# Kernel tuning notes

Hardware: AMD Instinct MI355X
Metric: run time of the kernel (lower is better)

Reference implementation:

```python
import jax, jax.numpy as jnp
import numpy as np

N_NODES = 100000
N_EDGES = 1000000
D = 64            # in_channels == heads*hidden_channels
OUT = 64          # out_channels
L = 3             # local_layers
RVQ = 3           # residual VQ levels per layer
CODES = 16
BN_EPS = 1e-5
COMMIT_W = 0.25


def _l2n(v, eps=1e-12):
    return v / (jnp.linalg.norm(v, axis=-1, keepdims=True) + eps)


def setup_inputs() -> dict:
    key = jax.random.key(0)
    ks = jax.random.split(key, 16)
    s = 1.0 / np.sqrt(D)
    inp = {
        "x": jax.random.normal(ks[0], (N_NODES, D), jnp.float32),
        "edge_index": jax.random.randint(ks[1], (2, N_EDGES), 0, N_NODES, jnp.int64),
        # SAGEConv: lin_l (applied to mean-aggregated neighbors, with bias), lin_r (root, no bias)
        "Wa": jax.random.uniform(ks[2], (L, D, D), jnp.float32, -s, s),
        "ba": jax.random.uniform(ks[3], (L, D), jnp.float32, -s, s),
        "Wr": jax.random.uniform(ks[4], (L, D, D), jnp.float32, -s, s),
        # skip Linear per layer
        "Wl": jax.random.uniform(ks[5], (L, D, D), jnp.float32, -s, s),
        "bl": jax.random.uniform(ks[6], (L, D), jnp.float32, -s, s),
        # BatchNorm affine
        "gamma": jnp.ones((L, D), jnp.float32),
        "beta": jnp.zeros((L, D), jnp.float32),
        # residual-VQ codebooks: [layer, rvq_level, codes, dim]
        "codebooks": jax.random.normal(ks[7], (L, RVQ, CODES, D), jnp.float32),
        # heads
        "Wp": jax.random.uniform(ks[8], (D, OUT), jnp.float32, -s, s),
        "bp": jax.random.uniform(ks[9], (OUT,), jnp.float32, -s, s),
        "Wg": jax.random.uniform(ks[10], (D, L * RVQ), jnp.float32, -s, s),
        "bg": jax.random.uniform(ks[11], (L * RVQ,), jnp.float32, -s, s),
    }
    return inp


def _sage_conv(x, src, dst, Wa, ba, Wr):
    # mean aggregation of source features onto destinations
    summed = jax.ops.segment_sum(x[src], dst, num_segments=N_NODES)
    cnt = jax.ops.segment_sum(jnp.ones((src.shape[0],), x.dtype), dst, num_segments=N_NODES)
    mean = summed / jnp.maximum(cnt, 1.0)[:, None]
    out = mean @ Wa + ba + x @ Wr
    return _l2n(out)  # normalize=True


def _residual_vq(x, cbs):
    # cosine-sim residual VQ, 3 levels; returns (quantized_sum, ids [N,RVQ], commit_loss)
    residual = x
    quant = jnp.zeros_like(x)
    loss = jnp.zeros((), x.dtype)
    ids = []
    for r in range(RVQ):
        cb = _l2n(cbs[r])                       # [CODES, D]
        sim = _l2n(residual) @ cb.T             # [N, CODES]
        idx = jnp.argmax(sim, axis=-1)          # [N]
        q = cb[idx]                             # [N, D]
        loss = loss + COMMIT_W * jnp.mean((jax.lax.stop_gradient(q) - residual) ** 2)
        q_st = residual + jax.lax.stop_gradient(q - residual)  # straight-through
        quant = quant + q_st
        residual = residual - jax.lax.stop_gradient(q)
        ids.append(idx)
    return quant, jnp.stack(ids, axis=1), loss


def reference(x, edge_index, Wa, ba, Wr, Wl, bl, gamma, beta, codebooks, Wp, bp, Wg, bg):
    src, dst = edge_index[0], edge_index[1]
    h = x  # in_dropout: identity at inference
    x_local = jnp.zeros((N_NODES, D), x.dtype)
    total_commit = jnp.zeros((), x.dtype)
    id_list = []
    for i in range(L):
        h = _sage_conv(h, src, dst, Wa[i], ba[i], Wr[i]) + (h @ Wl[i] + bl[i])
        # BatchNorm1d (batch statistics)
        mu = jnp.mean(h, axis=0)
        var = jnp.var(h, axis=0)
        h = (h - mu) * jax.lax.rsqrt(var + BN_EPS) * gamma[i] + beta[i]
        h = jax.nn.relu(h)  # dropout: identity at inference
        x_local = x_local + h
        _, ids, closs = _residual_vq(h, codebooks[i])
        total_commit = total_commit + closs
        id_list.append(ids)
    id_concat = jnp.concatenate(id_list, axis=1)  # [N, L*RVQ]
    gnn_id = x_local @ Wg + bg
    pred = x_local @ Wp + bp
    return (pred, total_commit, id_concat, gnn_id)
```

## Files before the change

### kernel.cpp

```cpp
#include <hip/hip_runtime.h>
#include <math.h>

#define NN 100000
#define NE 1000000
#define D 64
#define L 3
#define RVQ 3
#define CODES 16
#define BN_EPS 1e-5f
#define COMMIT_W 0.25f

#define GRID_A 2048

#define OFS_ROWPTR 0
#define OFS_CNT    100016
#define OFS_CURSOR 200032
#define OFS_BSUMS  300048
#define OFS_BOFFS  300176
#define OFS_STATS  300304
#define OFS_CSR    300800
#define OFS_HA     1300800
#define OFS_HB     7700800
#define OFS_XLOC   14100800
#define OFS_PART   20500800

#define OUT_PRED   0
#define OUT_COMMIT (NN * D)
#define OUT_IDS    (NN * D + 1)
#define OUT_GNN    (NN * D + 1 + NN * (L * RVQ))

static __device__ __forceinline__ float waveSum(float v) {
    #pragma unroll
    for (int off = 32; off; off >>= 1) v += __shfl_xor(v, off, 64);
    return v;
}

__global__ void k_count(const int* __restrict__ dst, int* __restrict__ cnt) {
    int e = blockIdx.x * blockDim.x + threadIdx.x;
    if (e < NE) atomicAdd(&cnt[dst[e]], 1);
}

#define SCAN_B 1024
__global__ void k_scan1(const int* __restrict__ cnt, int* __restrict__ rowptr,
                        int* __restrict__ bsums) {
    __shared__ int sm[SCAN_B];
    int t = threadIdx.x;
    int i = blockIdx.x * SCAN_B + t;
    int v = (i < NN) ? cnt[i] : 0;
    sm[t] = v;
    __syncthreads();
    for (int off = 1; off < SCAN_B; off <<= 1) {
        int add = (t >= off) ? sm[t - off] : 0;
        __syncthreads();
        sm[t] += add;
        __syncthreads();
    }
    if (i < NN) rowptr[i + 1] = sm[t];
    if (t == SCAN_B - 1) bsums[blockIdx.x] = sm[t];
}

__global__ void k_scan2(const int* __restrict__ bsums, int* __restrict__ boffs, int nb) {
    __shared__ int sm[SCAN_B];
    int t = threadIdx.x;
    int orig = (t < nb) ? bsums[t] : 0;
    sm[t] = orig;
    __syncthreads();
    for (int off = 1; off < SCAN_B; off <<= 1) {
        int add = (t >= off) ? sm[t - off] : 0;
        __syncthreads();
        sm[t] += add;
        __syncthreads();
    }
    if (t < nb) boffs[t] = sm[t] - orig;
}

__global__ void k_scan3(int* __restrict__ rowptr, const int* __restrict__ boffs) {
    int i = blockIdx.x * SCAN_B + threadIdx.x;
    if (i < NN) rowptr[i + 1] += boffs[blockIdx.x];
    if (i == 0) rowptr[0] = 0;
}

__global__ void k_cursor(const int* __restrict__ rowptr, int* __restrict__ cursor) {
    int i = blockIdx.x * blockDim.x + threadIdx.x;
    if (i < NN) cursor[i] = rowptr[i];
}

__global__ void k_fill(const int* __restrict__ src, const int* __restrict__ dst,
                       int* __restrict__ cursor, int* __restrict__ csr_src) {
    int e = blockIdx.x * blockDim.x + threadIdx.x;
    if (e < NE) {
        int p = atomicAdd(&cursor[dst[e]], 1);
        csr_src[p] = src[e];
    }
}

__global__ void k_sortrows(const int* __restrict__ rowptr, int* __restrict__ csr) {
    int n = blockIdx.x * blockDim.x + threadIdx.x;
    if (n >= NN) return;
    int r0 = rowptr[n], r1 = rowptr[n + 1];
    for (int i = r0 + 1; i < r1; ++i) {
        int v = csr[i];
        int j = i - 1;
        while (j >= r0 && csr[j] > v) { csr[j + 1] = csr[j]; --j; }
        csr[j + 1] = v;
    }
}

__global__ __launch_bounds__(256) void k_gather(
    const float* __restrict__ h, const int* __restrict__ rowptr,
    const int* __restrict__ csr_src, float* __restrict__ mean_out) {
    int t = threadIdx.x;
    int lane = t & 63, wid = t >> 6;
    int n = blockIdx.x * 4 + wid;
    if (n >= NN) return;

    int r0 = rowptr[n], r1 = rowptr[n + 1];
    float s = 0.f;
    for (int base = r0; base < r1; base += 64) {
        int last = r1 - 1;
        int ii = base + lane;
        int idx = csr_src[(ii <= last) ? ii : last];
        int m = r1 - base;
        if (m > 64) m = 64;
        int j = 0;
        for (; j + 8 <= m; j += 8) {
            int i0 = __shfl(idx, j + 0, 64), i1 = __shfl(idx, j + 1, 64);
            int i2 = __shfl(idx, j + 2, 64), i3 = __shfl(idx, j + 3, 64);
            int i4 = __shfl(idx, j + 4, 64), i5 = __shfl(idx, j + 5, 64);
            int i6 = __shfl(idx, j + 6, 64), i7 = __shfl(idx, j + 7, 64);
            float v0 = h[i0 * D + lane], v1 = h[i1 * D + lane];
            float v2 = h[i2 * D + lane], v3 = h[i3 * D + lane];
            float v4 = h[i4 * D + lane], v5 = h[i5 * D + lane];
            float v6 = h[i6 * D + lane], v7 = h[i7 * D + lane];
            s += v0; s += v1; s += v2; s += v3;
            s += v4; s += v5; s += v6; s += v7;
        }
        for (; j + 4 <= m; j += 4) {
            int i0 = __shfl(idx, j + 0, 64), i1 = __shfl(idx, j + 1, 64);
            int i2 = __shfl(idx, j + 2, 64), i3 = __shfl(idx, j + 3, 64);
            float v0 = h[i0 * D + lane], v1 = h[i1 * D + lane];
            float v2 = h[i2 * D + lane], v3 = h[i3 * D + lane];
            s += v0; s += v1; s += v2; s += v3;
        }
        for (; j < m; ++j) {
            int i0 = __shfl(idx, j, 64);
            s += h[i0 * D + lane];
        }
    }
    float deg = (float)(r1 - r0);
    mean_out[n * D + lane] = s / fmaxf(deg, 1.0f);
}

__global__ __launch_bounds__(256) void k_matvec(
    const float* __restrict__ h, float* __restrict__ hp,
    const float* __restrict__ Wa, const float* __restrict__ ba,
    const float* __restrict__ Wr, const float* __restrict__ Wl,
    const float* __restrict__ bl, float* __restrict__ partials) {
    __shared__ float red[2][4][D];
    __shared__ float lbuf[4][2][128];
    int t = threadIdx.x, lane = t & 63, wid = t >> 6;

    float wa[D], wr[D], wl[D];
    #pragma unroll
    for (int k = 0; k < D; ++k) {
        wa[k] = Wa[k * D + lane];
        wr[k] = Wr[k * D + lane];
        wl[k] = Wl[k * D + lane];
    }
    float bav = ba[lane], blv = bl[lane];

    int wg = blockIdx.x * 4 + wid;
    const int wstep = GRID_A * 4;
    float accS = 0.f, accQ = 0.f;

    int seg = lane >> 4;
    int sl  = lane & 15;

    {
        float4 v = {0.f, 0.f, 0.f, 0.f};
        if (seg == 0)      v = *(const float4*)(hp + (size_t)wg * D + 4 * sl);
        else if (seg == 1) v = *(const float4*)(h  + (size_t)wg * D + 4 * sl);
        if (seg < 2) *(float4*)&lbuf[wid][0][seg * 64 + 4 * sl] = v;
    }

    int p = 0;
    for (int n = wg; n < NN; n += wstep) {
        int nn = n + wstep;
        bool havepf = (nn < NN);
        float4 pf = {0.f, 0.f, 0.f, 0.f};
        if (havepf && seg < 2) {
            const float* srcp = (seg == 0) ? hp : h;
            pf = *(const float4*)(srcp + (size_t)nn * D + 4 * sl);
        }

        const float* mb = &lbuf[wid][p][0];
        const float* hb = &lbuf[wid][p][64];
        float a = 0.f, r = 0.f, lv = 0.f;
        #pragma unroll
        for (int j = 0; j < 16; ++j) {
            float4 m4 = *(const float4*)(mb + 4 * j);
            float4 h4 = *(const float4*)(hb + 4 * j);
            a += m4.x * wa[4 * j + 0]; r += h4.x * wr[4 * j + 0]; lv += h4.x * wl[4 * j + 0];
            a += m4.y * wa[4 * j + 1]; r += h4.y * wr[4 * j + 1]; lv += h4.y * wl[4 * j + 1];
            a += m4.z * wa[4 * j + 2]; r += h4.z * wr[4 * j + 2]; lv += h4.z * wl[4 * j + 2];
            a += m4.w * wa[4 * j + 3]; r += h4.w * wr[4 * j + 3]; lv += h4.w * wl[4 * j + 3];
        }
        float sage = a + bav + r;
        float ss = waveSum(sage * sage);
        float inv = 1.0f / (sqrtf(ss) + 1e-12f);
        float hpv = sage * inv + lv + blv;
        hp[(size_t)n * D + lane] = hpv;
        accS += hpv;
        accQ += hpv * hpv;

        if (havepf && seg < 2)
            *(float4*)&lbuf[wid][p ^ 1][seg * 64 + 4 * sl] = pf;
        p ^= 1;
    }

    red[0][wid][lane] = accS;
    red[1][wid][lane] = accQ;
    __syncthreads();
    if (wid == 0) {
        float s0 = (red[0][0][lane] + red[0][1][lane]) + (red[0][2][lane] + red[0][3][lane]);
        float q0 = (red[1][0][lane] + red[1][1][lane]) + (red[1][2][lane] + red[1][3][lane]);
        partials[blockIdx.x * 128 + lane]      = s0;
        partials[blockIdx.x * 128 + 64 + lane] = q0;
    }
}

__global__ __launch_bounds__(256) void k_red_stats(
    const float* __restrict__ part, float* __restrict__ stats) {
    __shared__ float sm[256];
    int c = blockIdx.x;
    int i = threadIdx.x;
    float s = 0.f;
    #pragma unroll
    for (int k = 0; k < 8; ++k)
        s += part[(size_t)(i * 8 + k) * 128 + c];
    sm[i] = s;
    __syncthreads();
    #pragma unroll
    for (int off = 128; off >= 1; off >>= 1) {
        if (i < off) sm[i] += sm[i + off];
        __syncthreads();
    }
    if (i == 0) stats[c] = sm[0];
}

#define CBSTRIDE 65
__global__ __launch_bounds__(256) void k_layer_b(
    float* __restrict__ hp,
    const float* __restrict__ stats,
    const float* __restrict__ gamma, const float* __restrict__ beta,
    const float* __restrict__ cbs,
    float* __restrict__ x_local,
    float* __restrict__ ids_out,
    int layer, float* __restrict__ commit, int first_layer) {
    __shared__ float scb[RVQ * CODES * CBSTRIDE];
    __shared__ float sres[256];
    __shared__ float sred[4];
    int t = threadIdx.x, lane = t & 63, wid = t >> 6;

    for (int row = wid; row < RVQ * CODES; row += 4) {
        float v = cbs[row * D + lane];
        float ss = waveSum(v * v);
        scb[row * CBSTRIDE + lane] = v / (sqrtf(ss) + 1e-12f);
    }
    __syncthreads();

    int jj = lane & 15, qq = lane >> 4;
    float cbr[RVQ][16];
    #pragma unroll
    for (int r = 0; r < RVQ; ++r)
        #pragma unroll
        for (int tt = 0; tt < 16; ++tt)
            cbr[r][tt] = scb[(r * CODES + jj) * CBSTRIDE + qq * 16 + tt];

    float mu = stats[lane] * (1.0f / NN);
    float var = stats[64 + lane] * (1.0f / NN) - mu * mu;
    float scale = rsqrtf(var + BN_EPS) * gamma[lane];
    float shift = beta[lane] - mu * scale;

    float closs = 0.f;
    int wg = blockIdx.x * 4 + wid;
    int wstep = gridDim.x * 4;

    for (int n = wg; n < NN; n += wstep) {
        float hpv = hp[n * D + lane];
        float hn = fmaxf(hpv * scale + shift, 0.f);
        hp[n * D + lane] = hn;
        if (first_layer) x_local[n * D + lane] = hn;
        else x_local[n * D + lane] += hn;

        float res = hn;
        int bis[RVQ];
        #pragma unroll
        for (int r = 0; r < RVQ; ++r) {
            sres[t] = res;
            float rc[16];
            #pragma unroll
            for (int i = 0; i < 4; ++i) {
                float4 v4 = *((const float4*)&sres[wid * 64 + qq * 16 + 4 * i]);
                rc[4 * i + 0] = v4.x; rc[4 * i + 1] = v4.y;
                rc[4 * i + 2] = v4.z; rc[4 * i + 3] = v4.w;
            }
            float p = 0.f;
            #pragma unroll
            for (int tt = 0; tt < 16; ++tt) p += rc[tt] * cbr[r][tt];
            p += __shfl_xor(p, 16, 64);
            p += __shfl_xor(p, 32, 64);
            float bv = p;
            int bi = jj;
            #pragma unroll
            for (int off = 8; off; off >>= 1) {
                float ov = __shfl_xor(bv, off, 64);
                int oi = __shfl_xor(bi, off, 64);
                if (ov > bv || (ov == bv && oi < bi)) { bv = ov; bi = oi; }
            }
            float q = scb[(r * CODES + bi) * CBSTRIDE + lane];
            float d = q - res;
            closs += d * d;
            res -= q;
            bis[r] = bi;
        }
        if (lane == 0) {
            ids_out[n * (L * RVQ) + layer * RVQ + 0] = (float)bis[0];
            ids_out[n * (L * RVQ) + layer * RVQ + 1] = (float)bis[1];
            ids_out[n * (L * RVQ) + layer * RVQ + 2] = (float)bis[2];
        }
    }

    closs = waveSum(closs);
    if (lane == 0) sred[wid] = closs;
    __syncthreads();
    if (t == 0) {
        float tot = (sred[0] + sred[1]) + (sred[2] + sred[3]);
        atomicAdd(commit, tot * (COMMIT_W / (float)(NN * D)));
    }
}

__global__ __launch_bounds__(256, 2) void k_head(
    const float* __restrict__ x_local,
    const float* __restrict__ Wp, const float* __restrict__ bp,
    const float* __restrict__ Wg, const float* __restrict__ bg,
    float* __restrict__ pred, float* __restrict__ gnn) {
    int t = threadIdx.x, lane = t & 63, wid = t >> 6;
    int jsafe = (lane < 9) ? lane : 0;

    float wp[D], wg[D];
    #pragma unroll
    for (int k = 0; k < D; ++k) {
        wp[k] = Wp[k * D + lane];
        wg[k] = Wg[k * 9 + jsafe];
    }
    float bpv = bp[lane], bgv = bg[jsafe];

    int w = blockIdx.x * 4 + wid;
    int wstep = gridDim.x * 4;
    for (int n = w; n < NN; n += wstep) {
        int nu = __builtin_amdgcn_readfirstlane(n);
        const float4* xrow = (const float4*)(x_local + (size_t)nu * D);
        float p = 0.f, g = 0.f;
        #pragma unroll
        for (int j = 0; j < 16; ++j) {
            float4 x4 = xrow[j];
            p += x4.x * wp[4 * j + 0]; g += x4.x * wg[4 * j + 0];
            p += x4.y * wp[4 * j + 1]; g += x4.y * wg[4 * j + 1];
            p += x4.z * wp[4 * j + 2]; g += x4.z * wg[4 * j + 2];
            p += x4.w * wp[4 * j + 3]; g += x4.w * wg[4 * j + 3];
        }
        pred[(size_t)n * D + lane] = p + bpv;
        if (lane < 9) gnn[(size_t)n * 9 + lane] = g + bgv;
    }
}

extern "C" void kernel_launch(void* const* d_in, const int* in_sizes, int n_in,
                              void* d_out, int out_size, void* d_ws, size_t ws_size,
                              hipStream_t stream) {
    const float* x   = (const float*)d_in[0];
    const int* ei    = (const int*)d_in[1];
    const float* Wa  = (const float*)d_in[2];
    const float* ba  = (const float*)d_in[3];
    const float* Wr  = (const float*)d_in[4];
    const float* Wl  = (const float*)d_in[5];
    const float* bl  = (const float*)d_in[6];
    const float* gamma = (const float*)d_in[7];
    const float* beta  = (const float*)d_in[8];
    const float* cbs = (const float*)d_in[9];
    const float* Wp  = (const float*)d_in[10];
    const float* bp  = (const float*)d_in[11];
    const float* Wg  = (const float*)d_in[12];
    const float* bg  = (const float*)d_in[13];

    const int* src = ei;
    const int* dst = ei + NE;

    int*   ws_i  = (int*)d_ws;
    float* ws_f  = (float*)d_ws;
    int* rowptr  = ws_i + OFS_ROWPTR;
    int* cnt     = ws_i + OFS_CNT;
    int* cursor  = ws_i + OFS_CURSOR;
    int* bsums   = ws_i + OFS_BSUMS;
    int* boffs   = ws_i + OFS_BOFFS;
    float* stats = ws_f + OFS_STATS;
    int* csr_src = ws_i + OFS_CSR;
    float* hA    = ws_f + OFS_HA;
    float* hB    = ws_f + OFS_HB;
    float* xloc  = ws_f + OFS_XLOC;
    float* part  = ws_f + OFS_PART;

    float* out    = (float*)d_out;
    float* pred   = out + OUT_PRED;
    float* commit = out + OUT_COMMIT;
    float* ids    = out + OUT_IDS;
    float* gnn    = out + OUT_GNN;

    hipMemsetAsync(cnt, 0, NN * sizeof(int), stream);
    hipMemsetAsync(commit, 0, sizeof(float), stream);

    k_count<<<(NE + 255) / 256, 256, 0, stream>>>(dst, cnt);
    int nscan = (NN + SCAN_B - 1) / SCAN_B;
    k_scan1<<<nscan, SCAN_B, 0, stream>>>(cnt, rowptr, bsums);
    k_scan2<<<1, SCAN_B, 0, stream>>>(bsums, boffs, nscan);
    k_scan3<<<nscan, SCAN_B, 0, stream>>>(rowptr, boffs);
    k_cursor<<<(NN + 1023) / 1024, 1024, 0, stream>>>(rowptr, cursor);
    k_fill<<<(NE + 255) / 256, 256, 0, stream>>>(src, dst, cursor, csr_src);
    k_sortrows<<<(NN + 255) / 256, 256, 0, stream>>>(rowptr, csr_src);

    const float* hin = x;
    float* bufs[2] = {hA, hB};
    for (int i = 0; i < L; ++i) {
        float* hp = bufs[i & 1];
        k_gather<<<(NN + 3) / 4, 256, 0, stream>>>(hin, rowptr, csr_src, hp);
        k_matvec<<<GRID_A, 256, 0, stream>>>(hin, hp,
                                             Wa + i * D * D, ba + i * D,
                                             Wr + i * D * D, Wl + i * D * D, bl + i * D,
                                             part);
        k_red_stats<<<128, 256, 0, stream>>>(part, stats + i * 128);
        k_layer_b<<<GRID_A, 256, 0, stream>>>(hp, stats + i * 128,
                                              gamma + i * D, beta + i * D,
                                              cbs + i * RVQ * CODES * D,
                                              xloc, ids, i, commit, (i == 0) ? 1 : 0);
        hin = hp;
    }

    k_head<<<2048, 256, 0, stream>>>(xloc, Wp, bp, Wg, bg, pred, gnn);
}
```

Before: 910.4 us.

## Defer BatchNorm+ReLU into consumers and drop x_local accumulation writes

The VQ kernel no longer writes the normalized activations back or accumulates x_local. Instead the BN affine and ReLU are recomputed on the fly in the next layer's gather and matvec, and in the head, which reads all three raw pre-BN buffers. This removes per-layer write and read-modify-write traffic of 100k x 64 floats. In exchange the gather pays an extra FMA and max per edge element, the head reads three buffers instead of one, and a third buffer is needed.

```diff
diff --git a/kernel.cpp b/kernel.cpp
--- a/kernel.cpp
+++ b/kernel.cpp
@@ -9,6 +9,7 @@
 #define CODES 16
 #define BN_EPS 1e-5f
 #define COMMIT_W 0.25f
+#define NEGINF -3.402823466e38f
 
 #define GRID_A 2048
 
@@ -21,7 +22,7 @@
 #define OFS_CSR    300800
 #define OFS_HA     1300800
 #define OFS_HB     7700800
-#define OFS_XLOC   14100800
+#define OFS_HC     14100800
 #define OFS_PART   20500800
 
 #define OUT_PRED   0
@@ -108,11 +109,22 @@
 
 __global__ __launch_bounds__(256) void k_gather(
     const float* __restrict__ h, const int* __restrict__ rowptr,
-    const int* __restrict__ csr_src, float* __restrict__ mean_out) {
+    const int* __restrict__ csr_src, float* __restrict__ mean_out,
+    const float* __restrict__ stats, const float* __restrict__ gamma,
+    const float* __restrict__ beta, int apply_bn) {
     int t = threadIdx.x;
     int lane = t & 63, wid = t >> 6;
     int n = blockIdx.x * 4 + wid;
     if (n >= NN) return;
+
+    float sc = 1.f, sh = 0.f, lim = NEGINF;
+    if (apply_bn) {
+        float mu = stats[lane] * (1.0f / NN);
+        float var = stats[64 + lane] * (1.0f / NN) - mu * mu;
+        sc = rsqrtf(var + BN_EPS) * gamma[lane];
+        sh = beta[lane] - mu * sc;
+        lim = 0.f;
+    }
 
     int r0 = rowptr[n], r1 = rowptr[n + 1];
     float s = 0.f;
@@ -132,6 +144,10 @@
             float v2 = h[i2 * D + lane], v3 = h[i3 * D + lane];
             float v4 = h[i4 * D + lane], v5 = h[i5 * D + lane];
             float v6 = h[i6 * D + lane], v7 = h[i7 * D + lane];
+            v0 = fmaxf(v0 * sc + sh, lim); v1 = fmaxf(v1 * sc + sh, lim);
+            v2 = fmaxf(v2 * sc + sh, lim); v3 = fmaxf(v3 * sc + sh, lim);
+            v4 = fmaxf(v4 * sc + sh, lim); v5 = fmaxf(v5 * sc + sh, lim);
+            v6 = fmaxf(v6 * sc + sh, lim); v7 = fmaxf(v7 * sc + sh, lim);
             s += v0; s += v1; s += v2; s += v3;
             s += v4; s += v5; s += v6; s += v7;
         }
@@ -140,11 +156,14 @@
             int i2 = __shfl(idx, j + 2, 64), i3 = __shfl(idx, j + 3, 64);
             float v0 = h[i0 * D + lane], v1 = h[i1 * D + lane];
             float v2 = h[i2 * D + lane], v3 = h[i3 * D + lane];
+            v0 = fmaxf(v0 * sc + sh, lim); v1 = fmaxf(v1 * sc + sh, lim);
+            v2 = fmaxf(v2 * sc + sh, lim); v3 = fmaxf(v3 * sc + sh, lim);
             s += v0; s += v1; s += v2; s += v3;
         }
         for (; j < m; ++j) {
             int i0 = __shfl(idx, j, 64);
-            s += h[i0 * D + lane];
+            float v0 = fmaxf(h[i0 * D + lane] * sc + sh, lim);
+            s += v0;
         }
     }
     float deg = (float)(r1 - r0);
@@ -155,7 +174,10 @@
     const float* __restrict__ h, float* __restrict__ hp,
     const float* __restrict__ Wa, const float* __restrict__ ba,
     const float* __restrict__ Wr, const float* __restrict__ Wl,
-    const float* __restrict__ bl, float* __restrict__ partials) {
+    const float* __restrict__ bl,
+    const float* __restrict__ stats, const float* __restrict__ gamma,
+    const float* __restrict__ beta, int apply_bn,
+    float* __restrict__ partials) {
     __shared__ float red[2][4][D];
     __shared__ float lbuf[4][2][128];
     int t = threadIdx.x, lane = t & 63, wid = t >> 6;
@@ -169,17 +191,35 @@
     }
     float bav = ba[lane], blv = bl[lane];
 
+    int seg = lane >> 4;
+    int sl  = lane & 15;
+
+    float sc0 = 1.f, sc1 = 1.f, sc2 = 1.f, sc3 = 1.f;
+    float sh0 = 0.f, sh1 = 0.f, sh2 = 0.f, sh3 = 0.f;
+    float lim = NEGINF;
+    if (apply_bn) {
+        int c = 4 * sl;
+        float mu, var, s_;
+        mu = stats[c+0]*(1.0f/NN); var = stats[64+c+0]*(1.0f/NN)-mu*mu; s_ = rsqrtf(var+BN_EPS)*gamma[c+0]; sc0 = s_; sh0 = beta[c+0]-mu*s_;
+        mu = stats[c+1]*(1.0f/NN); var = stats[64+c+1]*(1.0f/NN)-mu*mu; s_ = rsqrtf(var+BN_EPS)*gamma[c+1]; sc1 = s_; sh1 = beta[c+1]-mu*s_;
+        mu = stats[c+2]*(1.0f/NN); var = stats[64+c+2]*(1.0f/NN)-mu*mu; s_ = rsqrtf(var+BN_EPS)*gamma[c+2]; sc2 = s_; sh2 = beta[c+2]-mu*s_;
+        mu = stats[c+3]*(1.0f/NN); var = stats[64+c+3]*(1.0f/NN)-mu*mu; s_ = rsqrtf(var+BN_EPS)*gamma[c+3]; sc3 = s_; sh3 = beta[c+3]-mu*s_;
+        lim = 0.f;
+    }
+
     int wg = blockIdx.x * 4 + wid;
     const int wstep = GRID_A * 4;
     float accS = 0.f, accQ = 0.f;
 
-    int seg = lane >> 4;
-    int sl  = lane & 15;
-
     {
         float4 v = {0.f, 0.f, 0.f, 0.f};
-        if (seg == 0)      v = *(const float4*)(hp + (size_t)wg * D + 4 * sl);
-        else if (seg == 1) v = *(const float4*)(h  + (size_t)wg * D + 4 * sl);
+        if (seg == 0) {
+            v = *(const float4*)(hp + (size_t)wg * D + 4 * sl);
+        } else if (seg == 1) {
+            v = *(const float4*)(h + (size_t)wg * D + 4 * sl);
+            v.x = fmaxf(v.x * sc0 + sh0, lim); v.y = fmaxf(v.y * sc1 + sh1, lim);
+            v.z = fmaxf(v.z * sc2 + sh2, lim); v.w = fmaxf(v.w * sc3 + sh3, lim);
+        }
         if (seg < 2) *(float4*)&lbuf[wid][0][seg * 64 + 4 * sl] = v;
     }
 
@@ -189,8 +229,13 @@
         bool havepf = (nn < NN);
         float4 pf = {0.f, 0.f, 0.f, 0.f};
         if (havepf && seg < 2) {
-            const float* srcp = (seg == 0) ? hp : h;
-            pf = *(const float4*)(srcp + (size_t)nn * D + 4 * sl);
+            if (seg == 0) {
+                pf = *(const float4*)(hp + (size_t)nn * D + 4 * sl);
+            } else {
+                pf = *(const float4*)(h + (size_t)nn * D + 4 * sl);
+                pf.x = fmaxf(pf.x * sc0 + sh0, lim); pf.y = fmaxf(pf.y * sc1 + sh1, lim);
+                pf.z = fmaxf(pf.z * sc2 + sh2, lim); pf.w = fmaxf(pf.w * sc3 + sh3, lim);
+            }
         }
 
         const float* mb = &lbuf[wid][p][0];
@@ -249,14 +294,13 @@
 }
 
 #define CBSTRIDE 65
-__global__ __launch_bounds__(256) void k_layer_b(
-    float* __restrict__ hp,
+__global__ __launch_bounds__(256) void k_vq(
+    const float* __restrict__ hp,
     const float* __restrict__ stats,
     const float* __restrict__ gamma, const float* __restrict__ beta,
     const float* __restrict__ cbs,
-    float* __restrict__ x_local,
     float* __restrict__ ids_out,
-    int layer, float* __restrict__ commit, int first_layer) {
+    int layer, float* __restrict__ commit) {
     __shared__ float scb[RVQ * CODES * CBSTRIDE];
     __shared__ float sres[256];
     __shared__ float sred[4];
@@ -289,9 +333,6 @@
     for (int n = wg; n < NN; n += wstep) {
         float hpv = hp[n * D + lane];
         float hn = fmaxf(hpv * scale + shift, 0.f);
-        hp[n * D + lane] = hn;
-        if (first_layer) x_local[n * D + lane] = hn;
-        else x_local[n * D + lane] += hn;
 
         float res = hn;
         int bis[RVQ];
@@ -340,12 +381,17 @@
     }
 }
 
-__global__ __launch_bounds__(256, 2) void k_head(
-    const float* __restrict__ x_local,
+__global__ __launch_bounds__(256) void k_head(
+    const float* __restrict__ h0, const float* __restrict__ h1,
+    const float* __restrict__ h2,
+    const float* __restrict__ stats,
+    const float* __restrict__ gamma, const float* __restrict__ beta,
     const float* __restrict__ Wp, const float* __restrict__ bp,
     const float* __restrict__ Wg, const float* __restrict__ bg,
     float* __restrict__ pred, float* __restrict__ gnn) {
+    __shared__ float lbuf[4][2][64];
     int t = threadIdx.x, lane = t & 63, wid = t >> 6;
+    int seg = lane >> 4, sl = lane & 15;
     int jsafe = (lane < 9) ? lane : 0;
 
     float wp[D], wg[D];
@@ -356,15 +402,57 @@
     }
     float bpv = bp[lane], bgv = bg[jsafe];
 
-    int w = blockIdx.x * 4 + wid;
-    int wstep = gridDim.x * 4;
-    for (int n = w; n < NN; n += wstep) {
-        int nu = __builtin_amdgcn_readfirstlane(n);
-        const float4* xrow = (const float4*)(x_local + (size_t)nu * D);
+    float scv[12], shv[12];
+    #pragma unroll
+    for (int l = 0; l < 3; ++l) {
+        #pragma unroll
+        for (int e = 0; e < 4; ++e) {
+            int c = 4 * sl + e;
+            float mu = stats[l * 128 + c] * (1.0f / NN);
+            float var = stats[l * 128 + 64 + c] * (1.0f / NN) - mu * mu;
+            float s_ = rsqrtf(var + BN_EPS) * gamma[l * 64 + c];
+            scv[l * 4 + e] = s_;
+            shv[l * 4 + e] = beta[l * 64 + c] - mu * s_;
+        }
+    }
+
+    int wgi = blockIdx.x * 4 + wid;
+    const int wstep = 2048 * 4;
+
+    {
+        float4 x4 = {0.f, 0.f, 0.f, 0.f};
+        if (seg == 0) {
+            float4 a = *(const float4*)(h0 + (size_t)wgi * D + 4 * sl);
+            float4 b = *(const float4*)(h1 + (size_t)wgi * D + 4 * sl);
+            float4 c = *(const float4*)(h2 + (size_t)wgi * D + 4 * sl);
+            x4.x = (fmaxf(a.x*scv[0]+shv[0],0.f) + fmaxf(b.x*scv[4]+shv[4],0.f)) + fmaxf(c.x*scv[8]+shv[8],0.f);
+            x4.y = (fmaxf(a.y*scv[1]+shv[1],0.f) + fmaxf(b.y*scv[5]+shv[5],0.f)) + fmaxf(c.y*scv[9]+shv[9],0.f);
+            x4.z = (fmaxf(a.z*scv[2]+shv[2],0.f) + fmaxf(b.z*scv[6]+shv[6],0.f)) + fmaxf(c.z*scv[10]+shv[10],0.f);
+            x4.w = (fmaxf(a.w*scv[3]+shv[3],0.f) + fmaxf(b.w*scv[7]+shv[7],0.f)) + fmaxf(c.w*scv[11]+shv[11],0.f);
+            *(float4*)&lbuf[wid][0][4 * sl] = x4;
+        }
+    }
+
+    int par = 0;
+    for (int n = wgi; n < NN; n += wstep) {
+        int nn = n + wstep;
+        bool havepf = (nn < NN);
+        float4 pf = {0.f, 0.f, 0.f, 0.f};
+        if (havepf && seg == 0) {
+            float4 a = *(const float4*)(h0 + (size_t)nn * D + 4 * sl);
+            float4 b = *(const float4*)(h1 + (size_t)nn * D + 4 * sl);
+            float4 c = *(const float4*)(h2 + (size_t)nn * D + 4 * sl);
+            pf.x = (fmaxf(a.x*scv[0]+shv[0],0.f) + fmaxf(b.x*scv[4]+shv[4],0.f)) + fmaxf(c.x*scv[8]+shv[8],0.f);
+            pf.y = (fmaxf(a.y*scv[1]+shv[1],0.f) + fmaxf(b.y*scv[5]+shv[5],0.f)) + fmaxf(c.y*scv[9]+shv[9],0.f);
+            pf.z = (fmaxf(a.z*scv[2]+shv[2],0.f) + fmaxf(b.z*scv[6]+shv[6],0.f)) + fmaxf(c.z*scv[10]+shv[10],0.f);
+            pf.w = (fmaxf(a.w*scv[3]+shv[3],0.f) + fmaxf(b.w*scv[7]+shv[7],0.f)) + fmaxf(c.w*scv[11]+shv[11],0.f);
+        }
+
+        const float* xb = &lbuf[wid][par][0];
         float p = 0.f, g = 0.f;
         #pragma unroll
         for (int j = 0; j < 16; ++j) {
-            float4 x4 = xrow[j];
+            float4 x4 = *(const float4*)(xb + 4 * j);
             p += x4.x * wp[4 * j + 0]; g += x4.x * wg[4 * j + 0];
             p += x4.y * wp[4 * j + 1]; g += x4.y * wg[4 * j + 1];
             p += x4.z * wp[4 * j + 2]; g += x4.z * wg[4 * j + 2];
@@ -372,6 +460,10 @@
         }
         pred[(size_t)n * D + lane] = p + bpv;
         if (lane < 9) gnn[(size_t)n * 9 + lane] = g + bgv;
+
+        if (havepf && seg == 0)
+            *(float4*)&lbuf[wid][par ^ 1][4 * sl] = pf;
+        par ^= 1;
     }
 }
 
@@ -407,7 +499,7 @@
     int* csr_src = ws_i + OFS_CSR;
     float* hA    = ws_f + OFS_HA;
     float* hB    = ws_f + OFS_HB;
-    float* xloc  = ws_f + OFS_XLOC;
+    float* hC    = ws_f + OFS_HC;
     float* part  = ws_f + OFS_PART;
 
     float* out    = (float*)d_out;
@@ -429,21 +521,28 @@
     k_sortrows<<<(NN + 255) / 256, 256, 0, stream>>>(rowptr, csr_src);
 
     const float* hin = x;
-    float* bufs[2] = {hA, hB};
+    float* bufs[3] = {hA, hB, hC};
     for (int i = 0; i < L; ++i) {
-        float* hp = bufs[i & 1];
-        k_gather<<<(NN + 3) / 4, 256, 0, stream>>>(hin, rowptr, csr_src, hp);
+        float* hp = bufs[i];
+        const float* pstats = stats + (i > 0 ? (i - 1) * 128 : 0);
+        const float* pgamma = gamma + (i > 0 ? (i - 1) * D : 0);
+        const float* pbeta  = beta  + (i > 0 ? (i - 1) * D : 0);
+        int apply = (i > 0) ? 1 : 0;
+        k_gather<<<(NN + 3) / 4, 256, 0, stream>>>(hin, rowptr, csr_src, hp,
+                                                   pstats, pgamma, pbeta, apply);
         k_matvec<<<GRID_A, 256, 0, stream>>>(hin, hp,
                                              Wa + i * D * D, ba + i * D,
                                              Wr + i * D * D, Wl + i * D * D, bl + i * D,
+                                             pstats, pgamma, pbeta, apply,
                                              part);
         k_red_stats<<<128, 256, 0, stream>>>(part, stats + i * 128);
-        k_layer_b<<<GRID_A, 256, 0, stream>>>(hp, stats + i * 128,
-                                              gamma + i * D, beta + i * D,
-                                              cbs + i * RVQ * CODES * D,
-                                              xloc, ids, i, commit, (i == 0) ? 1 : 0);
+        k_vq<<<GRID_A, 256, 0, stream>>>(hp, stats + i * 128,
+                                         gamma + i * D, beta + i * D,
+                                         cbs + i * RVQ * CODES * D,
+                                         ids, i, commit);
         hin = hp;
     }
 
-    k_head<<<2048, 256, 0, stream>>>(xloc, Wp, bp, Wg, bg, pred, gnn);
-}
+    k_head<<<2048, 256, 0, stream>>>(hA, hB, hC, stats, gamma, beta,
+                                     Wp, bp, Wg, bg, pred, gnn);
+}
```

New measurement: 1.012 ms. 11.2% more time.

## Fuse neighbor mean-gather into the per-layer matvec kernel

Applied to the files above, without the earlier changes.

Merges the separate gather kernel, which wrote the mean-aggregated neighbor features to global memory, into the matvec kernel. Each wave now gathers the mean for its node, stages it in shared memory with the node's own features, and immediately applies the three weight projections. This removes one launch and a full write plus read of an N×64 intermediate per layer. In exchange, the gather now runs in a persistent grid of 2048 blocks whose waves each hold 192 weight registers, which lowers occupancy for the latency-bound random gather, and the double-buffered prefetch is dropped.

```diff
diff --git a/kernel.cpp b/kernel.cpp
--- a/kernel.cpp
+++ b/kernel.cpp
@@ -106,58 +106,15 @@
     }
 }
 
-__global__ __launch_bounds__(256) void k_gather(
+__global__ __launch_bounds__(256) void k_layer(
     const float* __restrict__ h, const int* __restrict__ rowptr,
-    const int* __restrict__ csr_src, float* __restrict__ mean_out) {
-    int t = threadIdx.x;
-    int lane = t & 63, wid = t >> 6;
-    int n = blockIdx.x * 4 + wid;
-    if (n >= NN) return;
-
-    int r0 = rowptr[n], r1 = rowptr[n + 1];
-    float s = 0.f;
-    for (int base = r0; base < r1; base += 64) {
-        int last = r1 - 1;
-        int ii = base + lane;
-        int idx = csr_src[(ii <= last) ? ii : last];
-        int m = r1 - base;
-        if (m > 64) m = 64;
-        int j = 0;
-        for (; j + 8 <= m; j += 8) {
-            int i0 = __shfl(idx, j + 0, 64), i1 = __shfl(idx, j + 1, 64);
-            int i2 = __shfl(idx, j + 2, 64), i3 = __shfl(idx, j + 3, 64);
-            int i4 = __shfl(idx, j + 4, 64), i5 = __shfl(idx, j + 5, 64);
-            int i6 = __shfl(idx, j + 6, 64), i7 = __shfl(idx, j + 7, 64);
-            float v0 = h[i0 * D + lane], v1 = h[i1 * D + lane];
-            float v2 = h[i2 * D + lane], v3 = h[i3 * D + lane];
-            float v4 = h[i4 * D + lane], v5 = h[i5 * D + lane];
-            float v6 = h[i6 * D + lane], v7 = h[i7 * D + lane];
-            s += v0; s += v1; s += v2; s += v3;
-            s += v4; s += v5; s += v6; s += v7;
-        }
-        for (; j + 4 <= m; j += 4) {
-            int i0 = __shfl(idx, j + 0, 64), i1 = __shfl(idx, j + 1, 64);
-            int i2 = __shfl(idx, j + 2, 64), i3 = __shfl(idx, j + 3, 64);
-            float v0 = h[i0 * D + lane], v1 = h[i1 * D + lane];
-            float v2 = h[i2 * D + lane], v3 = h[i3 * D + lane];
-            s += v0; s += v1; s += v2; s += v3;
-        }
-        for (; j < m; ++j) {
-            int i0 = __shfl(idx, j, 64);
-            s += h[i0 * D + lane];
-        }
-    }
-    float deg = (float)(r1 - r0);
-    mean_out[n * D + lane] = s / fmaxf(deg, 1.0f);
-}
-
-__global__ __launch_bounds__(256) void k_matvec(
-    const float* __restrict__ h, float* __restrict__ hp,
+    const int* __restrict__ csr_src, float* __restrict__ hp,
     const float* __restrict__ Wa, const float* __restrict__ ba,
     const float* __restrict__ Wr, const float* __restrict__ Wl,
-    const float* __restrict__ bl, float* __restrict__ partials) {
+    const float* __restrict__ bl,
+    float* __restrict__ partials) {
     __shared__ float red[2][4][D];
-    __shared__ float lbuf[4][2][128];
+    __shared__ float lbuf[4][128];
     int t = threadIdx.x, lane = t & 63, wid = t >> 6;
 
     float wa[D], wr[D], wl[D];
@@ -173,28 +130,49 @@
     const int wstep = GRID_A * 4;
     float accS = 0.f, accQ = 0.f;
 
-    int seg = lane >> 4;
-    int sl  = lane & 15;
-
-    {
-        float4 v = {0.f, 0.f, 0.f, 0.f};
-        if (seg == 0)      v = *(const float4*)(hp + (size_t)wg * D + 4 * sl);
-        else if (seg == 1) v = *(const float4*)(h  + (size_t)wg * D + 4 * sl);
-        if (seg < 2) *(float4*)&lbuf[wid][0][seg * 64 + 4 * sl] = v;
-    }
-
-    int p = 0;
     for (int n = wg; n < NN; n += wstep) {
-        int nn = n + wstep;
-        bool havepf = (nn < NN);
-        float4 pf = {0.f, 0.f, 0.f, 0.f};
-        if (havepf && seg < 2) {
-            const float* srcp = (seg == 0) ? hp : h;
-            pf = *(const float4*)(srcp + (size_t)nn * D + 4 * sl);
+        int r0 = rowptr[n], r1 = rowptr[n + 1];
+        float s = 0.f;
+        for (int base = r0; base < r1; base += 64) {
+            int last = r1 - 1;
+            int ii = base + lane;
+            int idx = csr_src[(ii <= last) ? ii : last];
+            int m = r1 - base;
+            if (m > 64) m = 64;
+            int j = 0;
+            for (; j + 8 <= m; j += 8) {
+                int i0 = __shfl(idx, j + 0, 64), i1 = __shfl(idx, j + 1, 64);
+                int i2 = __shfl(idx, j + 2, 64), i3 = __shfl(idx, j + 3, 64);
+                int i4 = __shfl(idx, j + 4, 64), i5 = __shfl(idx, j + 5, 64);
+                int i6 = __shfl(idx, j + 6, 64), i7 = __shfl(idx, j + 7, 64);
+                float v0 = h[i0 * D + lane], v1 = h[i1 * D + lane];
+                float v2 = h[i2 * D + lane], v3 = h[i3 * D + lane];
+                float v4 = h[i4 * D + lane], v5 = h[i5 * D + lane];
+                float v6 = h[i6 * D + lane], v7 = h[i7 * D + lane];
+                s += v0; s += v1; s += v2; s += v3;
+                s += v4; s += v5; s += v6; s += v7;
+            }
+            for (; j + 4 <= m; j += 4) {
+                int i0 = __shfl(idx, j + 0, 64), i1 = __shfl(idx, j + 1, 64);
+                int i2 = __shfl(idx, j + 2, 64), i3 = __shfl(idx, j + 3, 64);
+                float v0 = h[i0 * D + lane], v1 = h[i1 * D + lane];
+                float v2 = h[i2 * D + lane], v3 = h[i3 * D + lane];
+                s += v0; s += v1; s += v2; s += v3;
+            }
+            for (; j < m; ++j) {
+                int i0 = __shfl(idx, j, 64);
+                s += h[i0 * D + lane];
+            }
         }
-
-        const float* mb = &lbuf[wid][p][0];
-        const float* hb = &lbuf[wid][p][64];
+        float deg = (float)(r1 - r0);
+        float mean = s / fmaxf(deg, 1.0f);
+        float hv = h[(size_t)n * D + lane];
+
+        lbuf[wid][lane] = mean;
+        lbuf[wid][64 + lane] = hv;
+
+        const float* mb = &lbuf[wid][0];
+        const float* hb = &lbuf[wid][64];
         float a = 0.f, r = 0.f, lv = 0.f;
         #pragma unroll
         for (int j = 0; j < 16; ++j) {
@@ -212,10 +190,6 @@
         hp[(size_t)n * D + lane] = hpv;
         accS += hpv;
         accQ += hpv * hpv;
-
-        if (havepf && seg < 2)
-            *(float4*)&lbuf[wid][p ^ 1][seg * 64 + 4 * sl] = pf;
-        p ^= 1;
     }
 
     red[0][wid][lane] = accS;
@@ -432,11 +406,10 @@
     float* bufs[2] = {hA, hB};
     for (int i = 0; i < L; ++i) {
         float* hp = bufs[i & 1];
-        k_gather<<<(NN + 3) / 4, 256, 0, stream>>>(hin, rowptr, csr_src, hp);
-        k_matvec<<<GRID_A, 256, 0, stream>>>(hin, hp,
-                                             Wa + i * D * D, ba + i * D,
-                                             Wr + i * D * D, Wl + i * D * D, bl + i * D,
-                                             part);
+        k_layer<<<GRID_A, 256, 0, stream>>>(hin, rowptr, csr_src, hp,
+                                            Wa + i * D * D, ba + i * D,
+                                            Wr + i * D * D, Wl + i * D * D, bl + i * D,
+                                            part);
         k_red_stats<<<128, 256, 0, stream>>>(part, stats + i * 128);
         k_layer_b<<<GRID_A, 256, 0, stream>>>(hp, stats + i * 128,
                                               gamma + i * D, beta + i * D,
```

Result: slower. 1.048 ms (+15.1%).
